# Optimization experiments

Measured on AMD Instinct MI355X. Metric: run time of the kernel, lower is better.

The kernel has to match this reference:

```python
import jax, jax.numpy as jnp
import numpy as np

B, G, N1, S1 = 2, 16, 4096, 1024
D1, D2 = 128, 256
IN_CH = D1 + D2
MLP = [256, 256]
EPS_DIST = 1e-8
EPS_BN = 1e-5


def setup_inputs() -> dict:
    key = jax.random.key(0)
    ks = jax.random.split(key, 6)
    return {
        "xyz1": jax.random.normal(ks[0], (B, 3, G * N1), jnp.float32),
        "points1": jax.random.normal(ks[1], (B, D1, G * N1), jnp.float32),
        "point_split1": jnp.arange(G + 1, dtype=jnp.int32) * N1,
        "xyz2": jax.random.normal(ks[2], (B, 3, G * S1), jnp.float32),
        "points2": jax.random.normal(ks[3], (B, D2, G * S1), jnp.float32),
        "point_split2": jnp.arange(G + 1, dtype=jnp.int32) * S1,
        "W1": jax.random.normal(ks[4], (MLP[0], IN_CH), jnp.float32) / np.sqrt(IN_CH).astype(np.float32),
        "b1": jnp.zeros((MLP[0],), jnp.float32),
        "gamma1": jnp.ones((MLP[0],), jnp.float32),
        "beta1": jnp.zeros((MLP[0],), jnp.float32),
        "W2": jax.random.normal(ks[5], (MLP[1], MLP[0]), jnp.float32) / np.sqrt(MLP[0]).astype(np.float32),
        "b2": jnp.zeros((MLP[1],), jnp.float32),
        "gamma2": jnp.ones((MLP[1],), jnp.float32),
        "beta2": jnp.zeros((MLP[1],), jnp.float32),
    }


def _bn_relu(x, gamma, beta):
    # training-mode BatchNorm1d over (batch, points) per channel; x: [B, C, N]
    mu = x.mean(axis=(0, 2), keepdims=True)
    var = x.var(axis=(0, 2), keepdims=True)  # biased var, as torch training BN
    xn = (x - mu) * jax.lax.rsqrt(var + EPS_BN)
    return jax.nn.relu(xn * gamma[None, :, None] + beta[None, :, None])


def _fp_segment(x1, x2, p1, p2, W1, b1, g1, be1, W2, b2, g2, be2):
    # x1 [B,3,n], x2 [B,3,s], p1 [B,D1,n], p2 [B,D2,s]
    d = jnp.sum((x1[:, :, :, None] - x2[:, :, None, :]) ** 2, axis=1)  # [B,n,s]
    negd, idx = jax.lax.top_k(-d, 3)  # 3 nearest neighbors
    w = 1.0 / (-negd + EPS_DIST)
    w = w / jnp.sum(w, axis=-1, keepdims=True)  # [B,n,3]

    def gather(p2b, ixb, wb):  # [D2,s], [n,3], [n,3] -> [D2,n]
        return jnp.einsum('dnk,nk->dn', p2b[:, ixb], wb)

    interp = jax.vmap(gather)(p2, idx, w)  # [B,D2,n]
    h = jnp.concatenate([p1, interp], axis=1)  # [B,IN_CH,n]
    h = _bn_relu(jnp.einsum('oc,bcn->bon', W1, h) + b1[None, :, None], g1, be1)
    h = _bn_relu(jnp.einsum('oc,bcn->bon', W2, h) + b2[None, :, None], g2, be2)
    return h  # [B, MLP[-1], n]


def _forward(xyz1, points1, xyz2, points2, W1, b1, gamma1, beta1, W2, b2, gamma2, beta2, g):
    n1 = xyz1.shape[-1] // g
    s1 = xyz2.shape[-1] // g
    seg = lambda t, L: jnp.moveaxis(t.reshape(t.shape[0], t.shape[1], g, L), 2, 0)  # -> [G,B,C,L]
    out = jax.vmap(_fp_segment, in_axes=(0, 0, 0, 0) + (None,) * 8)(
        seg(xyz1, n1), seg(xyz2, s1), seg(points1, n1), seg(points2, s1),
        W1, b1, gamma1, beta1, W2, b2, gamma2, beta2)  # [G,B,C,n1]
    return jnp.moveaxis(out, 0, 2).reshape(out.shape[1], out.shape[2], g * n1)  # [B,C,N]


def reference(xyz1, points1, point_split1, xyz2, points2, point_split2,
              W1, b1, gamma1, beta1, W2, b2, gamma2, beta2):
    g = point_split1.shape[0] - 1  # number of ragged segments (uniform here)
    return _forward(xyz1, points1, xyz2, points2, W1, b1, gamma1, beta1,
                    W2, b2, gamma2, beta2, g)
```

## Files before the change

kernel.cpp:

```cpp
#include <hip/hip_runtime.h>
#include <hip/hip_bf16.h>
#include <hip/hip_fp16.h>

#define B_    2
#define G_    16
#define N_    4096
#define S_    1024
#define D1_   128
#define D2_   256
#define CIN_  384
#define BG_   32
#define GN_   65536
#define GS_   16384

typedef unsigned int u32;
typedef unsigned short u16;
typedef _Float16 f16x8 __attribute__((ext_vector_type(8)));
typedef float f32x4 __attribute__((ext_vector_type(4)));

__device__ __forceinline__ u32 h2bits(__half2 h) { union { __half2 h; u32 u; } c; c.h = h; return c.u; }
__device__ __forceinline__ __half2 bits2h(u32 u) { union { __half2 h; u32 u; } c; c.u = u; return c.h; }
__device__ __forceinline__ u32 pkmax0(u32 v) {
  u32 r; asm("v_pk_max_f16 %0, %1, %2" : "=v"(r) : "v"(v), "v"(0)); return r;
}
__device__ __forceinline__ void g2l16(const u16* g, u16* l) {
  __builtin_amdgcn_global_load_lds((const __attribute__((address_space(1))) u32*)g,
                                   (__attribute__((address_space(3))) u32*)l, 16, 0, 0);
}

#define OFF_W1H    0u
#define OFF_W2H    196608u
#define OFF_XYZ2P  327680u
#define OFF_SUM1   851968u
#define OFF_SQ1    868352u
#define OFF_SUM2   884736u
#define OFF_SQ2    901120u
#define OFF_SCPK1  917504u
#define OFF_SHPK1  925696u
#define OFF_SS2    950272u
#define OFF_KNNP   983040u
#define OFF_P2T    5177344u
#define OFF_Y2     21954560u
#define OFF_Y1     122617856u

__launch_bounds__(256)
__global__ void prep_kernel(const float* __restrict__ W1, const float* __restrict__ W2,
                            const float* __restrict__ xyz2,
                            u16* __restrict__ W1h, u16* __restrict__ W2h,
                            float4* __restrict__ xyz2p, float* __restrict__ zeros)
{
  int idx = blockIdx.x * 256 + threadIdx.x;
  if (idx < 98304) { W1h[idx] = __half_as_ushort(__float2half_rn(W1[idx])); return; }
  idx -= 98304;
  if (idx < 65536) { W2h[idx] = __half_as_ushort(__float2half_rn(W2[idx])); return; }
  idx -= 65536;
  if (idx < 16384) { zeros[idx] = 0.f; return; }
  idx -= 16384;
  int bg = idx >> 8, q = idx & 255;
  int b = bg >> 4, g = bg & 15;
  const float* base = xyz2 + (size_t)b * 3 * GS_ + (size_t)g * S_ + q * 4;
  float4 X = *(const float4*)(base);
  float4 Y = *(const float4*)(base + GS_);
  float4 Z = *(const float4*)(base + 2 * GS_);
  float4 M;
  M.x = X.x*X.x + Y.x*Y.x + Z.x*Z.x;
  M.y = X.y*X.y + Y.y*Y.y + Z.y*Z.y;
  M.z = X.z*X.z + Y.z*Y.z + Z.z*Z.z;
  M.w = X.w*X.w + Y.w*Y.w + Z.w*Z.w;
  float4* dst = xyz2p + (size_t)idx * 4;
  dst[0] = X; dst[1] = Y; dst[2] = Z; dst[3] = M;
}

__launch_bounds__(256)
__global__ void t2_kernel(const float* __restrict__ p2, u16* __restrict__ p2T)
{
  __shared__ float tl[64][65];
  int bx = blockIdx.x;
  int bg = bx >> 6, r = bx & 63;
  int ct = r >> 4, st = r & 15;
  int c0 = ct * 64, s0 = st * 64;
  int b = bg >> 4, g = bg & 15;
  int t = threadIdx.x, lane = t & 63, w = t >> 6;
  const float* src = p2 + (size_t)b * D2_ * GS_ + (size_t)g * S_ + s0 + lane;
  #pragma unroll
  for (int i = 0; i < 16; i++) {
    int row = w * 16 + i;
    tl[row][lane] = src[(size_t)(c0 + row) * GS_];
  }
  __syncthreads();
  int cp = t & 31, sr = t >> 5;
  #pragma unroll
  for (int i = 0; i < 8; i++) {
    int sl = sr * 8 + i;
    u32 v = h2bits(__floats2half2_rn(tl[2 * cp][sl], tl[2 * cp + 1][sl]));
    *(u32*)(p2T + (((size_t)bg * 1024 + s0 + sl) * 256 + c0 + 2 * cp)) = v;
  }
}

__launch_bounds__(256)
__global__ void knn_kernel(const float* __restrict__ xyz1, const float4* __restrict__ xyz2p,
                           uint4* __restrict__ knnp)
{
  __shared__ float sd[3][256];
  __shared__ int si[3][256];
  int bx = blockIdx.x;
  int bg = bx >> 6, blk = bx & 63;
  int b = bg >> 4, g = bg & 15;
  int t = threadIdx.x;
  int lane = t & 63, w = t >> 6;
  int n = blk * 64 + lane;
  const float* x1b = xyz1 + (size_t)b * 3 * GN_ + (size_t)g * N_ + n;
  float x = x1b[0], y = x1b[GN_], z = x1b[2 * GN_];
  const float4* xp = xyz2p + (size_t)bg * 1024;

  float d0 = 3.4e38f, d1 = 3.4e38f, d2 = 3.4e38f;
  int i0 = 0, i1 = 0, i2 = 0;
  for (int qq = 0; qq < 64; qq++) {
    int q = w * 64 + qq;
    float4 X = xp[q * 4 + 0], Y = xp[q * 4 + 1], Z = xp[q * 4 + 2], M = xp[q * 4 + 3];
    const float* Xa = (const float*)&X;
    const float* Ya = (const float*)&Y;
    const float* Za = (const float*)&Z;
    const float* Ma = (const float*)&M;
    #pragma unroll
    for (int u = 0; u < 4; u++) {
      float cr = x * Xa[u];
      cr = fmaf(y, Ya[u], cr);
      cr = fmaf(z, Za[u], cr);
      float d = fmaf(-2.f, cr, Ma[u]);
      int s = q * 4 + u;
      bool c2 = d < d2, c1 = d < d1, c0 = d < d0;
      d2 = c1 ? d1 : (c2 ? d : d2);  i2 = c1 ? i1 : (c2 ? s : i2);
      d1 = c0 ? d0 : (c1 ? d : d1);  i1 = c0 ? i0 : (c1 ? s : i1);
      d0 = c0 ? d : d0;              i0 = c0 ? s : i0;
    }
  }

  sd[0][t] = d0; sd[1][t] = d1; sd[2][t] = d2;
  si[0][t] = i0; si[1][t] = i1; si[2][t] = i2;
  __syncthreads();

  if (t < 64) {
    float D0 = d0, D1 = d1, D2 = d2;
    int I0 = i0, I1 = i1, I2 = i2;
    #pragma unroll
    for (int qtr = 1; qtr < 4; qtr++) {
      int idx = qtr * 64 + t;
      #pragma unroll
      for (int c = 0; c < 3; c++) {
        float d = sd[c][idx];
        int s = si[c][idx];
        bool c0 = d < D0, c1 = d < D1, c2 = d < D2;
        I2 = c1 ? I1 : (c2 ? s : I2);  D2 = c1 ? D1 : (c2 ? d : D2);
        I1 = c0 ? I0 : (c1 ? s : I1);  D1 = c0 ? D0 : (c1 ? d : D1);
        I0 = c0 ? s : I0;              D0 = c0 ? d : D0;
      }
    }
    float m1 = x * x + y * y + z * z;
    float t0 = fmaxf(D0 + m1, 0.f), t1 = fmaxf(D1 + m1, 0.f), t2v = fmaxf(D2 + m1, 0.f);
    float w0 = 1.f / (t0 + 1e-8f);
    float w1 = 1.f / (t1 + 1e-8f);
    float w2 = 1.f / (t2v + 1e-8f);
    float inv = 1.f / (w0 + w1 + w2);
    uint4 rec;
    rec.x = h2bits(__floats2half2_rn(w0 * inv, w1 * inv));
    rec.y = (u32)__half_as_ushort(__float2half_rn(w2 * inv));
    rec.z = (u32)I0 | ((u32)I1 << 16);
    rec.w = (u32)I2;
    knnp[(size_t)bg * 4096 + n] = rec;
  }
}

__launch_bounds__(256, 2)
__global__ void gemm1_kernel(const u16* __restrict__ W1h, const float* __restrict__ points1,
                             const u16* __restrict__ p2T, const uint4* __restrict__ knnp,
                             const float* __restrict__ bias,
                             float* __restrict__ sumw, float* __restrict__ sqw,
                             u16* __restrict__ Y1)
{
  __shared__ __align__(16) char smem[81920];
  int bx = blockIdx.x;
  int bg = bx >> 6, nt = bx & 63;
  int b = bg >> 4, g = bg & 15;
  int n0 = nt * 64;
  int t = threadIdx.x, wid = t >> 6, l = t & 63;
  int llo = l & 15, lhi = l >> 4;

  {
    int half = l >> 5, cl = l & 31;
    size_t kb = (size_t)bg * 4096 + n0;
    const u16* p2b = p2T + (size_t)bg * 1024 * 256;
    #pragma unroll
    for (int p = 0; p < 8; p++) {
      int r = wid * 16 + p * 2 + half;
      uint4 kp = knnp[kb + r];
      __half2 w0 = __half2half2(__low2half(bits2h(kp.x)));
      __half2 w1 = __half2half2(__high2half(bits2h(kp.x)));
      __half2 w2 = __half2half2(__low2half(bits2h(kp.y)));
      int i0 = kp.z & 0xffff, i1 = kp.z >> 16, i2 = kp.w & 0xffff;
      uint4 q0 = *(const uint4*)(p2b + (size_t)i0 * 256 + cl * 8);
      uint4 q1 = *(const uint4*)(p2b + (size_t)i1 * 256 + cl * 8);
      uint4 q2 = *(const uint4*)(p2b + (size_t)i2 * 256 + cl * 8);
      const u32* a0 = (const u32*)&q0;
      const u32* a1 = (const u32*)&q1;
      const u32* a2 = (const u32*)&q2;
      uint4 o;
      u32* ow = (u32*)&o;
      #pragma unroll
      for (int w = 0; w < 4; w++) {
        __half2 v = __hmul2(w2, bits2h(a2[w]));
        v = __hfma2(w1, bits2h(a1[w]), v);
        v = __hfma2(w0, bits2h(a0[w]), v);
        ow[w] = h2bits(v);
      }
      *(uint4*)(smem + r * 768 + ((256 + cl * 16) ^ ((r & 15) << 4))) = o;
    }
    const float* p1c = points1 + ((size_t)b * 128 + wid * 32) * (size_t)GN_
                     + (size_t)g * N_ + n0 + l;
    #pragma unroll
    for (int cp = 0; cp < 16; cp++) {
      int c = wid * 32 + cp * 2;
      u32 pk = h2bits(__floats2half2_rn(p1c[(size_t)(cp * 2) * GN_],
                                        p1c[(size_t)(cp * 2 + 1) * GN_]));
      *(u32*)(smem + l * 768 + ((c * 2) ^ ((l & 15) << 4))) = pk;
    }
  }

  auto stageA = [&](int ks) {
    u16* dst = (u16*)(smem + 49152 + (ks & 1) * 16384);
    #pragma unroll
    for (int q = 0; q < 4; q++) {
      int idx = q * 256 + t;
      g2l16(W1h + (size_t)(idx >> 2) * 384 + ks * 32 + (idx & 3) * 8,
            dst + (q * 256 + wid * 64) * 8);
    }
  };

  stageA(0);
  __syncthreads();

  f32x4 acc[4][4];
  #pragma unroll
  for (int i = 0; i < 4; i++)
    #pragma unroll
    for (int j = 0; j < 4; j++) acc[i][j] = (f32x4)0.f;

  for (int ks = 0; ks < 12; ks++) {
    if (ks < 11) stageA(ks + 1);
    const char* Ab = smem + 49152 + (ks & 1) * 16384;
    f16x8 bfr[4], afr[4];
    #pragma unroll
    for (int j = 0; j < 4; j++) {
      int rb = j * 16 + llo;
      bfr[j] = *(const f16x8*)(smem + rb * 768 + ((ks * 64 + lhi * 16) ^ ((rb & 15) << 4)));
    }
    #pragma unroll
    for (int i = 0; i < 4; i++)
      afr[i] = *(const f16x8*)(Ab + (wid * 64 + i * 16 + llo) * 64 + lhi * 16);
    #pragma unroll
    for (int i = 0; i < 4; i++)
      #pragma unroll
      for (int j = 0; j < 4; j++)
        acc[i][j] = __builtin_amdgcn_mfma_f32_16x16x32_f16(afr[i], bfr[j], acc[i][j], 0, 0, 0);
    __syncthreads();
  }

  #pragma unroll
  for (int i = 0; i < 4; i++) {
    int mloc = wid * 64 + i * 16 + lhi * 4;
    float b0 = bias[mloc], b1 = bias[mloc + 1], b2 = bias[mloc + 2], b3 = bias[mloc + 3];
    float s0 = 0, s1 = 0, s2 = 0, s3 = 0, q0 = 0, q1 = 0, q2 = 0, q3 = 0;
    int slotb = (mloc * 2) & ~15, off8 = (mloc * 2) & 15;
    #pragma unroll
    for (int j = 0; j < 4; j++) {
      int n = j * 16 + llo;
      float v0 = acc[i][j][0] + b0;
      float v1 = acc[i][j][1] + b1;
      float v2 = acc[i][j][2] + b2;
      float v3 = acc[i][j][3] + b3;
      s0 += v0; q0 += v0 * v0;
      s1 += v1; q1 += v1 * v1;
      s2 += v2; q2 += v2 * v2;
      s3 += v3; q3 += v3 * v3;
      int base = n * 512 + (slotb ^ ((n & 7) << 4)) + off8;
      *(u32*)(smem + 49152 + base) = h2bits(__floats2half2_rn(v0, v1));
      *(u32*)(smem + 49152 + base + 4) = h2bits(__floats2half2_rn(v2, v3));
    }
    #pragma unroll
    for (int off = 1; off < 16; off <<= 1) {
      s0 += __shfl_xor(s0, off, 64); q0 += __shfl_xor(q0, off, 64);
      s1 += __shfl_xor(s1, off, 64); q1 += __shfl_xor(q1, off, 64);
      s2 += __shfl_xor(s2, off, 64); q2 += __shfl_xor(q2, off, 64);
      s3 += __shfl_xor(s3, off, 64); q3 += __shfl_xor(q3, off, 64);
    }
    if (llo == 0) {
      atomicAdd(&sumw[g * 256 + mloc], s0);     atomicAdd(&sqw[g * 256 + mloc], q0);
      atomicAdd(&sumw[g * 256 + mloc + 1], s1); atomicAdd(&sqw[g * 256 + mloc + 1], q1);
      atomicAdd(&sumw[g * 256 + mloc + 2], s2); atomicAdd(&sqw[g * 256 + mloc + 2], q2);
      atomicAdd(&sumw[g * 256 + mloc + 3], s3); atomicAdd(&sqw[g * 256 + mloc + 3], q3);
    }
  }
  __syncthreads();
  {
    int rn = t >> 2, cq = t & 3;
    u16* yrow = Y1 + ((size_t)bg * 4096 + n0 + rn) * 256;
    #pragma unroll
    for (int u = 0; u < 8; u++) {
      int s = u * 4 + cq;
      uint4 v = *(const uint4*)(smem + 49152 + rn * 512 + ((s * 16) ^ ((rn & 7) << 4)));
      *(uint4*)(yrow + s * 8) = v;
    }
  }
}

__global__ void bnfin_kernel(const float* __restrict__ sum, const float* __restrict__ sq,
                             const float* __restrict__ gamma, const float* __restrict__ beta,
                             float2* __restrict__ ss, u32* __restrict__ scpk, u32* __restrict__ shpk)
{
  __shared__ float scl[256], shl[256];
  int g = blockIdx.x, m = threadIdx.x;
  int i = g * 256 + m;
  float mean = sum[i] * (1.f / 8192.f);
  float var = sq[i] * (1.f / 8192.f) - mean * mean;
  var = fmaxf(var, 0.f);
  float rstd = rsqrtf(var + 1e-5f);
  float sc = gamma[m] * rstd;
  float sh = beta[m] - mean * sc;
  if (ss) ss[i] = make_float2(sc, sh);
  if (scpk) {
    scl[m] = sc; shl[m] = sh;
    __syncthreads();
    if (m < 128) {
      scpk[g * 128 + m] = h2bits(__floats2half2_rn(scl[2 * m], scl[2 * m + 1]));
      shpk[g * 128 + m] = h2bits(__floats2half2_rn(shl[2 * m], shl[2 * m + 1]));
    }
  }
}

__launch_bounds__(256, 2)
__global__ void gemm2_kernel(const u16* __restrict__ W2h, const u16* __restrict__ Y1,
                             const u32* __restrict__ scpk, const u32* __restrict__ shpk,
                             const float* __restrict__ bias,
                             float* __restrict__ sumw, float* __restrict__ sqw,
                             u16* __restrict__ Y2)
{
  __shared__ __align__(16) char smem[66560];
  int bx = blockIdx.x;
  int bg = bx >> 6, nt = bx & 63;
  int b = bg >> 4, g = bg & 15;
  int n0 = nt * 64;
  int t = threadIdx.x, wid = t >> 6, l = t & 63;
  int llo = l & 15, lhi = l >> 4;

  if (t < 128) {
    *(u32*)(smem + 65536 + t * 4) = scpk[g * 128 + t];
    *(u32*)(smem + 66048 + t * 4) = shpk[g * 128 + t];
  }

  {
    int rn = t >> 2, qq = t & 3;
    const u16* yrow = Y1 + ((size_t)bg * 4096 + n0 + rn) * 256 + qq * 64;
    uint4 sreg[8];
    #pragma unroll
    for (int u = 0; u < 8; u++) sreg[u] = *(const uint4*)(yrow + u * 8);
    __syncthreads();
    const u32* scp = (const u32*)(smem + 65536);
    const u32* shp = (const u32*)(smem + 66048);
    #pragma unroll
    for (int u = 0; u < 8; u++) {
      int s = qq * 8 + u;
      const u32* yw = (const u32*)&sreg[u];
      uint4 o;
      u32* ow = (u32*)&o;
      #pragma unroll
      for (int w = 0; w < 4; w++) {
        int pairi = qq * 32 + u * 4 + w;
        __half2 v = __hfma2(bits2h(yw[w]), bits2h(scp[pairi]), bits2h(shp[pairi]));
        ow[w] = pkmax0(h2bits(v));
      }
      *(uint4*)(smem + rn * 512 + ((s * 16) ^ ((rn & 15) << 4))) = o;
    }
  }

  auto stageA = [&](int ks) {
    u16* dst = (u16*)(smem + 32768 + (ks & 1) * 16384);
    #pragma unroll
    for (int q = 0; q < 4; q++) {
      int idx = q * 256 + t;
      g2l16(W2h + (size_t)(idx >> 2) * 256 + ks * 32 + (idx & 3) * 8,
            dst + (q * 256 + wid * 64) * 8);
    }
  };

  stageA(0);
  __syncthreads();

  f32x4 acc[4][4];
  #pragma unroll
  for (int i = 0; i < 4; i++)
    #pragma unroll
    for (int j = 0; j < 4; j++) acc[i][j] = (f32x4)0.f;

  for (int ks = 0; ks < 8; ks++) {
    if (ks < 7) stageA(ks + 1);
    const char* Ab = smem + 32768 + (ks & 1) * 16384;
    f16x8 bfr[4], afr[4];
    #pragma unroll
    for (int j = 0; j < 4; j++) {
      int rb = j * 16 + llo;
      bfr[j] = *(const f16x8*)(smem + rb * 512 + ((ks * 64 + lhi * 16) ^ ((rb & 15) << 4)));
    }
    #pragma unroll
    for (int i = 0; i < 4; i++)
      afr[i] = *(const f16x8*)(Ab + (wid * 64 + i * 16 + llo) * 64 + lhi * 16);
    #pragma unroll
    for (int i = 0; i < 4; i++)
      #pragma unroll
      for (int j = 0; j < 4; j++)
        acc[i][j] = __builtin_amdgcn_mfma_f32_16x16x32_f16(afr[i], bfr[j], acc[i][j], 0, 0, 0);
    __syncthreads();
  }

  #pragma unroll
  for (int i = 0; i < 4; i++) {
    int mloc = wid * 64 + i * 16 + lhi * 4;
    float b0 = bias[mloc], b1 = bias[mloc + 1], b2 = bias[mloc + 2], b3 = bias[mloc + 3];
    float s0 = 0, s1 = 0, s2 = 0, s3 = 0, q0 = 0, q1 = 0, q2 = 0, q3 = 0;
    #pragma unroll
    for (int j = 0; j < 4; j++) {
      int n = j * 16 + llo;
      int slotn = (n >> 3) * 16, offn = (n * 2) & 15;
      float v0 = acc[i][j][0] + b0;
      float v1 = acc[i][j][1] + b1;
      float v2 = acc[i][j][2] + b2;
      float v3 = acc[i][j][3] + b3;
      s0 += v0; q0 += v0 * v0;
      s1 += v1; q1 += v1 * v1;
      s2 += v2; q2 += v2 * v2;
      s3 += v3; q3 += v3 * v3;
      *(u16*)(smem + 32768 + (mloc + 0) * 128 + (slotn ^ (((mloc + 0) & 7) << 4)) + offn) =
          __half_as_ushort(__float2half_rn(v0));
      *(u16*)(smem + 32768 + (mloc + 1) * 128 + (slotn ^ (((mloc + 1) & 7) << 4)) + offn) =
          __half_as_ushort(__float2half_rn(v1));
      *(u16*)(smem + 32768 + (mloc + 2) * 128 + (slotn ^ (((mloc + 2) & 7) << 4)) + offn) =
          __half_as_ushort(__float2half_rn(v2));
      *(u16*)(smem + 32768 + (mloc + 3) * 128 + (slotn ^ (((mloc + 3) & 7) << 4)) + offn) =
          __half_as_ushort(__float2half_rn(v3));
    }
    #pragma unroll
    for (int off = 1; off < 16; off <<= 1) {
      s0 += __shfl_xor(s0, off, 64); q0 += __shfl_xor(q0, off, 64);
      s1 += __shfl_xor(s1, off, 64); q1 += __shfl_xor(q1, off, 64);
      s2 += __shfl_xor(s2, off, 64); q2 += __shfl_xor(q2, off, 64);
      s3 += __shfl_xor(s3, off, 64); q3 += __shfl_xor(q3, off, 64);
    }
    if (llo == 0) {
      atomicAdd(&sumw[g * 256 + mloc], s0);     atomicAdd(&sqw[g * 256 + mloc], q0);
      atomicAdd(&sumw[g * 256 + mloc + 1], s1); atomicAdd(&sqw[g * 256 + mloc + 1], q1);
      atomicAdd(&sumw[g * 256 + mloc + 2], s2); atomicAdd(&sqw[g * 256 + mloc + 2], q2);
      atomicAdd(&sumw[g * 256 + mloc + 3], s3); atomicAdd(&sqw[g * 256 + mloc + 3], q3);
    }
  }
  __syncthreads();
  {
    int rr = t >> 2, cq = t & 3;
    #pragma unroll
    for (int p = 0; p < 4; p++) {
      int mr = p * 64 + rr;
      u16* yrow = Y2 + ((size_t)b * 256 + mr) * (size_t)GN_ + (size_t)g * N_ + n0;
      #pragma unroll
      for (int u = 0; u < 2; u++) {
        int s = cq * 2 + u;
        uint4 v = *(const uint4*)(smem + 32768 + mr * 128 + ((s * 16) ^ ((mr & 7) << 4)));
        *(uint4*)(yrow + s * 8) = v;
      }
    }
  }
}

__launch_bounds__(256)
__global__ void bnapply2_kernel(const u16* __restrict__ Y2, const float2* __restrict__ ss,
                                float* __restrict__ Out)
{
  int f8 = blockIdx.x * 256 + threadIdx.x;
  size_t base = (size_t)f8 * 8;
  int m = (int)((base >> 16) & 255);
  int g = (int)((base >> 12) & 15);
  float2 sc = ss[g * 256 + m];
  uint4 yv = *(const uint4*)(Y2 + base);
  const u32* yw = (const u32*)&yv;
  float4 a, b4;
  float* av = (float*)&a;
  float* bvv = (float*)&b4;
  #pragma unroll
  for (int i = 0; i < 2; i++) {
    float2 f = __half22float2(bits2h(yw[i]));
    av[2 * i]     = fmaxf(fmaf(f.x, sc.x, sc.y), 0.f);
    av[2 * i + 1] = fmaxf(fmaf(f.y, sc.x, sc.y), 0.f);
  }
  #pragma unroll
  for (int i = 0; i < 2; i++) {
    float2 f = __half22float2(bits2h(yw[2 + i]));
    bvv[2 * i]     = fmaxf(fmaf(f.x, sc.x, sc.y), 0.f);
    bvv[2 * i + 1] = fmaxf(fmaf(f.y, sc.x, sc.y), 0.f);
  }
  *(float4*)(Out + base) = a;
  *(float4*)(Out + base + 4) = b4;
}

extern "C" void kernel_launch(void* const* d_in, const int* in_sizes, int n_in,
                              void* d_out, int out_size, void* d_ws, size_t ws_size,
                              hipStream_t stream)
{
  (void)in_sizes; (void)n_in; (void)out_size; (void)ws_size;
  const float* xyz1    = (const float*)d_in[0];
  const float* points1 = (const float*)d_in[1];
  const float* xyz2    = (const float*)d_in[3];
  const float* points2 = (const float*)d_in[4];
  const float* W1      = (const float*)d_in[6];
  const float* b1      = (const float*)d_in[7];
  const float* gamma1  = (const float*)d_in[8];
  const float* beta1   = (const float*)d_in[9];
  const float* W2      = (const float*)d_in[10];
  const float* b2      = (const float*)d_in[11];
  const float* gamma2  = (const float*)d_in[12];
  const float* beta2   = (const float*)d_in[13];
  float* out = (float*)d_out;
  char* ws = (char*)d_ws;

  u16*    W1h   = (u16*)(ws + OFF_W1H);
  u16*    W2h   = (u16*)(ws + OFF_W2H);
  float4* xyz2p = (float4*)(ws + OFF_XYZ2P);
  float*  sum1  = (float*)(ws + OFF_SUM1);
  float*  sq1   = (float*)(ws + OFF_SQ1);
  float*  sum2  = (float*)(ws + OFF_SUM2);
  float*  sq2   = (float*)(ws + OFF_SQ2);
  u32*    scpk1 = (u32*)(ws + OFF_SCPK1);
  u32*    shpk1 = (u32*)(ws + OFF_SHPK1);
  float2* ss2   = (float2*)(ws + OFF_SS2);
  uint4*  knnp  = (uint4*)(ws + OFF_KNNP);
  u16*    p2T   = (u16*)(ws + OFF_P2T);
  u16*    Y2    = (u16*)(ws + OFF_Y2);
  u16*    Y1    = (u16*)(ws + OFF_Y1);

  prep_kernel<<<736, 256, 0, stream>>>(W1, W2, xyz2, W1h, W2h, xyz2p, sum1);
  t2_kernel<<<2048, 256, 0, stream>>>(points2, p2T);
  knn_kernel<<<2048, 256, 0, stream>>>(xyz1, xyz2p, knnp);
  gemm1_kernel<<<2048, 256, 0, stream>>>(W1h, points1, p2T, knnp, b1, sum1, sq1, Y1);
  bnfin_kernel<<<16, 256, 0, stream>>>(sum1, sq1, gamma1, beta1, nullptr, scpk1, shpk1);
  gemm2_kernel<<<2048, 256, 0, stream>>>(W2h, Y1, scpk1, shpk1, b2, sum2, sq2, Y2);
  bnfin_kernel<<<16, 256, 0, stream>>>(sum2, sq2, gamma2, beta2, ss2, nullptr, nullptr);
  bnapply2_kernel<<<16384, 256, 0, stream>>>(Y2, ss2, out);
}
```

Before: 278.2 us.

## Prepack weights in MFMA fragment order and load A directly from global

The prep kernel now writes W1 and W2 in fp16, packed in the per-lane MFMA fragment order. The GEMM kernels then load A fragments straight from global memory (L2-resident) instead of double-buffering them through LDS with global_load_lds. This drops the per-k-step barrier and cuts LDS use, so launch bounds rise to 3 blocks per SM for higher occupancy. The cost is that global-load latency now sits inside the MFMA loop with no software prefetch.

```diff
diff --git a/kernel.cpp b/kernel.cpp
--- a/kernel.cpp
+++ b/kernel.cpp
@@ -23,13 +23,9 @@
 __device__ __forceinline__ u32 pkmax0(u32 v) {
   u32 r; asm("v_pk_max_f16 %0, %1, %2" : "=v"(r) : "v"(v), "v"(0)); return r;
 }
-__device__ __forceinline__ void g2l16(const u16* g, u16* l) {
-  __builtin_amdgcn_global_load_lds((const __attribute__((address_space(1))) u32*)g,
-                                   (__attribute__((address_space(3))) u32*)l, 16, 0, 0);
-}
-
-#define OFF_W1H    0u
-#define OFF_W2H    196608u
+
+#define OFF_W1PK   0u
+#define OFF_W2PK   196608u
 #define OFF_XYZ2P  327680u
 #define OFF_SUM1   851968u
 #define OFF_SQ1    868352u
@@ -46,14 +42,30 @@
 __launch_bounds__(256)
 __global__ void prep_kernel(const float* __restrict__ W1, const float* __restrict__ W2,
                             const float* __restrict__ xyz2,
-                            u16* __restrict__ W1h, u16* __restrict__ W2h,
+                            u16* __restrict__ W1pk, u16* __restrict__ W2pk,
                             float4* __restrict__ xyz2p, float* __restrict__ zeros)
 {
   int idx = blockIdx.x * 256 + threadIdx.x;
-  if (idx < 98304) { W1h[idx] = __half_as_ushort(__float2half_rn(W1[idx])); return; }
-  idx -= 98304;
-  if (idx < 65536) { W2h[idx] = __half_as_ushort(__float2half_rn(W2[idx])); return; }
-  idx -= 65536;
+  if (idx < 12288) {
+    int lane = idx & 63, ks = (idx >> 6) % 12, mr = idx / (64 * 12);
+    int m = mr * 16 + (lane & 15), k = ks * 32 + (lane >> 4) * 8;
+    const float* src = W1 + (size_t)m * 384 + k;
+    u16* dst = W1pk + (size_t)idx * 8;
+    #pragma unroll
+    for (int e = 0; e < 8; e++) dst[e] = __half_as_ushort(__float2half_rn(src[e]));
+    return;
+  }
+  idx -= 12288;
+  if (idx < 8192) {
+    int lane = idx & 63, ks = (idx >> 6) % 8, mr = idx / (64 * 8);
+    int m = mr * 16 + (lane & 15), k = ks * 32 + (lane >> 4) * 8;
+    const float* src = W2 + (size_t)m * 256 + k;
+    u16* dst = W2pk + (size_t)idx * 8;
+    #pragma unroll
+    for (int e = 0; e < 8; e++) dst[e] = __half_as_ushort(__float2half_rn(src[e]));
+    return;
+  }
+  idx -= 8192;
   if (idx < 16384) { zeros[idx] = 0.f; return; }
   idx -= 16384;
   int bg = idx >> 8, q = idx & 255;
@@ -171,14 +183,14 @@
   }
 }
 
-__launch_bounds__(256, 2)
-__global__ void gemm1_kernel(const u16* __restrict__ W1h, const float* __restrict__ points1,
+__launch_bounds__(256, 3)
+__global__ void gemm1_kernel(const u16* __restrict__ W1pk, const float* __restrict__ points1,
                              const u16* __restrict__ p2T, const uint4* __restrict__ knnp,
                              const float* __restrict__ bias,
                              float* __restrict__ sumw, float* __restrict__ sqw,
                              u16* __restrict__ Y1)
 {
-  __shared__ __align__(16) char smem[81920];
+  __shared__ __align__(16) char smem[49152];
   int bx = blockIdx.x;
   int bg = bx >> 6, nt = bx & 63;
   int b = bg >> 4, g = bg & 15;
@@ -225,18 +237,6 @@
       *(u32*)(smem + l * 768 + ((c * 2) ^ ((l & 15) << 4))) = pk;
     }
   }
-
-  auto stageA = [&](int ks) {
-    u16* dst = (u16*)(smem + 49152 + (ks & 1) * 16384);
-    #pragma unroll
-    for (int q = 0; q < 4; q++) {
-      int idx = q * 256 + t;
-      g2l16(W1h + (size_t)(idx >> 2) * 384 + ks * 32 + (idx & 3) * 8,
-            dst + (q * 256 + wid * 64) * 8);
-    }
-  };
-
-  stageA(0);
   __syncthreads();
 
   f32x4 acc[4][4];
@@ -246,8 +246,6 @@
     for (int j = 0; j < 4; j++) acc[i][j] = (f32x4)0.f;
 
   for (int ks = 0; ks < 12; ks++) {
-    if (ks < 11) stageA(ks + 1);
-    const char* Ab = smem + 49152 + (ks & 1) * 16384;
     f16x8 bfr[4], afr[4];
     #pragma unroll
     for (int j = 0; j < 4; j++) {
@@ -256,14 +254,14 @@
     }
     #pragma unroll
     for (int i = 0; i < 4; i++)
-      afr[i] = *(const f16x8*)(Ab + (wid * 64 + i * 16 + llo) * 64 + lhi * 16);
+      afr[i] = *(const f16x8*)(W1pk + (size_t)(((wid * 4 + i) * 12 + ks) * 64 + l) * 8);
     #pragma unroll
     for (int i = 0; i < 4; i++)
       #pragma unroll
       for (int j = 0; j < 4; j++)
         acc[i][j] = __builtin_amdgcn_mfma_f32_16x16x32_f16(afr[i], bfr[j], acc[i][j], 0, 0, 0);
-    __syncthreads();
-  }
+  }
+  __syncthreads();
 
   #pragma unroll
   for (int i = 0; i < 4; i++) {
@@ -283,8 +281,8 @@
       s2 += v2; q2 += v2 * v2;
       s3 += v3; q3 += v3 * v3;
       int base = n * 512 + (slotb ^ ((n & 7) << 4)) + off8;
-      *(u32*)(smem + 49152 + base) = h2bits(__floats2half2_rn(v0, v1));
-      *(u32*)(smem + 49152 + base + 4) = h2bits(__floats2half2_rn(v2, v3));
+      *(u32*)(smem + base) = h2bits(__floats2half2_rn(v0, v1));
+      *(u32*)(smem + base + 4) = h2bits(__floats2half2_rn(v2, v3));
     }
     #pragma unroll
     for (int off = 1; off < 16; off <<= 1) {
@@ -307,7 +305,7 @@
     #pragma unroll
     for (int u = 0; u < 8; u++) {
       int s = u * 4 + cq;
-      uint4 v = *(const uint4*)(smem + 49152 + rn * 512 + ((s * 16) ^ ((rn & 7) << 4)));
+      uint4 v = *(const uint4*)(smem + rn * 512 + ((s * 16) ^ ((rn & 7) << 4)));
       *(uint4*)(yrow + s * 8) = v;
     }
   }
@@ -337,14 +335,14 @@
   }
 }
 
-__launch_bounds__(256, 2)
-__global__ void gemm2_kernel(const u16* __restrict__ W2h, const u16* __restrict__ Y1,
+__launch_bounds__(256, 3)
+__global__ void gemm2_kernel(const u16* __restrict__ W2pk, const u16* __restrict__ Y1,
                              const u32* __restrict__ scpk, const u32* __restrict__ shpk,
                              const float* __restrict__ bias,
                              float* __restrict__ sumw, float* __restrict__ sqw,
                              u16* __restrict__ Y2)
 {
-  __shared__ __align__(16) char smem[66560];
+  __shared__ __align__(16) char smem[33792];
   int bx = blockIdx.x;
   int bg = bx >> 6, nt = bx & 63;
   int b = bg >> 4, g = bg & 15;
@@ -353,8 +351,8 @@
   int llo = l & 15, lhi = l >> 4;
 
   if (t < 128) {
-    *(u32*)(smem + 65536 + t * 4) = scpk[g * 128 + t];
-    *(u32*)(smem + 66048 + t * 4) = shpk[g * 128 + t];
+    *(u32*)(smem + 32768 + t * 4) = scpk[g * 128 + t];
+    *(u32*)(smem + 33280 + t * 4) = shpk[g * 128 + t];
   }
 
   {
@@ -364,8 +362,8 @@
     #pragma unroll
     for (int u = 0; u < 8; u++) sreg[u] = *(const uint4*)(yrow + u * 8);
     __syncthreads();
-    const u32* scp = (const u32*)(smem + 65536);
-    const u32* shp = (const u32*)(smem + 66048);
+    const u32* scp = (const u32*)(smem + 32768);
+    const u32* shp = (const u32*)(smem + 33280);
     #pragma unroll
     for (int u = 0; u < 8; u++) {
       int s = qq * 8 + u;
@@ -381,18 +379,6 @@
       *(uint4*)(smem + rn * 512 + ((s * 16) ^ ((rn & 15) << 4))) = o;
     }
   }
-
-  auto stageA = [&](int ks) {
-    u16* dst = (u16*)(smem + 32768 + (ks & 1) * 16384);
-    #pragma unroll
-    for (int q = 0; q < 4; q++) {
-      int idx = q * 256 + t;
-      g2l16(W2h + (size_t)(idx >> 2) * 256 + ks * 32 + (idx & 3) * 8,
-            dst + (q * 256 + wid * 64) * 8);
-    }
-  };
-
-  stageA(0);
   __syncthreads();
 
   f32x4 acc[4][4];
@@ -402,8 +388,6 @@
     for (int j = 0; j < 4; j++) acc[i][j] = (f32x4)0.f;
 
   for (int ks = 0; ks < 8; ks++) {
-    if (ks < 7) stageA(ks + 1);
-    const char* Ab = smem + 32768 + (ks & 1) * 16384;
     f16x8 bfr[4], afr[4];
     #pragma unroll
     for (int j = 0; j < 4; j++) {
@@ -412,14 +396,14 @@
     }
     #pragma unroll
     for (int i = 0; i < 4; i++)
-      afr[i] = *(const f16x8*)(Ab + (wid * 64 + i * 16 + llo) * 64 + lhi * 16);
+      afr[i] = *(const f16x8*)(W2pk + (size_t)(((wid * 4 + i) * 8 + ks) * 64 + l) * 8);
     #pragma unroll
     for (int i = 0; i < 4; i++)
       #pragma unroll
       for (int j = 0; j < 4; j++)
         acc[i][j] = __builtin_amdgcn_mfma_f32_16x16x32_f16(afr[i], bfr[j], acc[i][j], 0, 0, 0);
-    __syncthreads();
-  }
+  }
+  __syncthreads();
 
   #pragma unroll
   for (int i = 0; i < 4; i++) {
@@ -438,13 +422,13 @@
       s1 += v1; q1 += v1 * v1;
       s2 += v2; q2 += v2 * v2;
       s3 += v3; q3 += v3 * v3;
-      *(u16*)(smem + 32768 + (mloc + 0) * 128 + (slotn ^ (((mloc + 0) & 7) << 4)) + offn) =
+      *(u16*)(smem + (mloc + 0) * 128 + (slotn ^ (((mloc + 0) & 7) << 4)) + offn) =
           __half_as_ushort(__float2half_rn(v0));
-      *(u16*)(smem + 32768 + (mloc + 1) * 128 + (slotn ^ (((mloc + 1) & 7) << 4)) + offn) =
+      *(u16*)(smem + (mloc + 1) * 128 + (slotn ^ (((mloc + 1) & 7) << 4)) + offn) =
           __half_as_ushort(__float2half_rn(v1));
-      *(u16*)(smem + 32768 + (mloc + 2) * 128 + (slotn ^ (((mloc + 2) & 7) << 4)) + offn) =
+      *(u16*)(smem + (mloc + 2) * 128 + (slotn ^ (((mloc + 2) & 7) << 4)) + offn) =
           __half_as_ushort(__float2half_rn(v2));
-      *(u16*)(smem + 32768 + (mloc + 3) * 128 + (slotn ^ (((mloc + 3) & 7) << 4)) + offn) =
+      *(u16*)(smem + (mloc + 3) * 128 + (slotn ^ (((mloc + 3) & 7) << 4)) + offn) =
           __half_as_ushort(__float2half_rn(v3));
     }
     #pragma unroll
@@ -471,7 +455,7 @@
       #pragma unroll
       for (int u = 0; u < 2; u++) {
         int s = cq * 2 + u;
-        uint4 v = *(const uint4*)(smem + 32768 + mr * 128 + ((s * 16) ^ ((mr & 7) << 4)));
+        uint4 v = *(const uint4*)(smem + mr * 128 + ((s * 16) ^ ((mr & 7) << 4)));
         *(uint4*)(yrow + s * 8) = v;
       }
     }
@@ -528,8 +512,8 @@
   float* out = (float*)d_out;
   char* ws = (char*)d_ws;
 
-  u16*    W1h   = (u16*)(ws + OFF_W1H);
-  u16*    W2h   = (u16*)(ws + OFF_W2H);
+  u16*    W1pk  = (u16*)(ws + OFF_W1PK);
+  u16*    W2pk  = (u16*)(ws + OFF_W2PK);
   float4* xyz2p = (float4*)(ws + OFF_XYZ2P);
   float*  sum1  = (float*)(ws + OFF_SUM1);
   float*  sq1   = (float*)(ws + OFF_SQ1);
@@ -543,12 +527,12 @@
   u16*    Y2    = (u16*)(ws + OFF_Y2);
   u16*    Y1    = (u16*)(ws + OFF_Y1);
 
-  prep_kernel<<<736, 256, 0, stream>>>(W1, W2, xyz2, W1h, W2h, xyz2p, sum1);
+  prep_kernel<<<176, 256, 0, stream>>>(W1, W2, xyz2, W1pk, W2pk, xyz2p, sum1);
   t2_kernel<<<2048, 256, 0, stream>>>(points2, p2T);
   knn_kernel<<<2048, 256, 0, stream>>>(xyz1, xyz2p, knnp);
-  gemm1_kernel<<<2048, 256, 0, stream>>>(W1h, points1, p2T, knnp, b1, sum1, sq1, Y1);
+  gemm1_kernel<<<2048, 256, 0, stream>>>(W1pk, points1, p2T, knnp, b1, sum1, sq1, Y1);
   bnfin_kernel<<<16, 256, 0, stream>>>(sum1, sq1, gamma1, beta1, nullptr, scpk1, shpk1);
-  gemm2_kernel<<<2048, 256, 0, stream>>>(W2h, Y1, scpk1, shpk1, b2, sum2, sq2, Y2);
+  gemm2_kernel<<<2048, 256, 0, stream>>>(W2pk, Y1, scpk1, shpk1, b2, sum2, sq2, Y2);
   bnfin_kernel<<<16, 256, 0, stream>>>(sum2, sq2, gamma2, beta2, ss2, nullptr, nullptr);
   bnapply2_kernel<<<16384, 256, 0, stream>>>(Y2, ss2, out);
 }
```

Result: faster. 258.9 us (-7.0%).
